# Optimization experiments

Hardware: AMD Instinct MI355X
Metric: run time of the kernel (lower is better)

Reference implementation:

```python
import jax, jax.numpy as jnp
import numpy as np

FILTER_LENGTH = 800
HOP_LENGTH = 200
WIN_LENGTH = 800
NUM_SAMPLES = 8_000_000


def _make_forward_basis():
    # Real/imag DFT rows (cutoff = N/2+1) times a periodic Hamming window.
    fl, wl = FILTER_LENGTH, WIN_LENGTH
    fourier = np.fft.fft(np.eye(fl))
    cutoff = fl // 2 + 1  # 401
    basis = np.vstack([fourier[:cutoff].real, fourier[:cutoff].imag])  # [802, 800]
    n = np.arange(wl)
    window = 0.54 - 0.46 * np.cos(2.0 * np.pi * n / wl)  # scipy get_window('hamming', wl, fftbins=True)
    basis = basis * window[None, :]
    return jnp.asarray(basis[:, None, :], dtype=jnp.float32)  # [802, 1, 800] (OIH)


def setup_inputs() -> dict:
    key = jax.random.key(0)
    input_data = jax.random.normal(key, (NUM_SAMPLES,), dtype=jnp.float32)
    forward_basis = _make_forward_basis()
    return {"input_data": input_data, "forward_basis": forward_basis}


def reference(input_data, forward_basis):
    fl, hop = FILTER_LENGTH, HOP_LENGTH
    cutoff = fl // 2 + 1
    x = input_data.reshape(1, 1, -1)  # (N=1, C=1, T)
    x = jnp.pad(x, ((0, 0), (0, 0), (fl // 2, fl // 2)), mode='reflect')
    # Strided conv with the dense DFT basis == framed windowed DFT.
    out = jax.lax.conv_general_dilated(
        x, forward_basis, window_strides=(hop,), padding='VALID',
        dimension_numbers=('NCH', 'OIH', 'NCH'))  # [1, 802, n_frames]
    real = out[:, :cutoff, :]
    imag = out[:, cutoff:, :]
    magnitude = jnp.sqrt(real * real + imag * imag)  # [1, 401, n_frames]
    return magnitude
```

## Files before the change

kernel.cpp:

```cpp
#include <hip/hip_runtime.h>


#define FL   800
#define HOP  200
#define CUT  401
#define NS   8000000
#define NT   40001
#define KSTEPS 25

#define FT   64
#define TT   384
#define NTT  105
#define SLICE_SH 77824
#define XBN  8016000
#define BB_OFF 16032000

typedef short short8 __attribute__((ext_vector_type(8)));
typedef float float4v __attribute__((ext_vector_type(4)));

#define GU32 const __attribute__((address_space(1))) unsigned int*
#define LU32 __attribute__((address_space(3))) unsigned int*

__device__ inline unsigned short f2bf(float f) {
    union { float f; unsigned u; } v; v.f = f;
    unsigned r = v.u + 0x7FFFu + ((v.u >> 16) & 1u);
    return (unsigned short)(r >> 16);
}

__global__ void prep_x(const float* __restrict__ x, short* __restrict__ xb) {
    const int n8 = XBN / 8;
    for (int j = blockIdx.x * blockDim.x + threadIdx.x; j < n8;
         j += gridDim.x * blockDim.x) {
        const int i = j * 8;
        const int s = i - 400;
        short8 o;
        if (s >= 0 && s + 7 < NS) {
            const float4v a = *reinterpret_cast<const float4v*>(x + s);
            const float4v b = *reinterpret_cast<const float4v*>(x + s + 4);
            o[0]=f2bf(a[0]); o[1]=f2bf(a[1]); o[2]=f2bf(a[2]); o[3]=f2bf(a[3]);
            o[4]=f2bf(b[0]); o[5]=f2bf(b[1]); o[6]=f2bf(b[2]); o[7]=f2bf(b[3]);
        } else {
            #pragma unroll
            for (int q = 0; q < 8; ++q) {
                int sq = s + q;
                if (sq < 0) sq = -sq;
                else if (sq >= NS) sq = 2 * NS - 2 - sq;
                o[q] = f2bf(x[sq]);
            }
        }
        *reinterpret_cast<short8*>(xb + i) = o;
    }
}

__global__ void prep_b(const float* __restrict__ basis, short* __restrict__ bb) {
    const int nch = 896 * 100;
    for (int j = blockIdx.x * blockDim.x + threadIdx.x; j < nch;
         j += gridDim.x * blockDim.x) {
        const int row = j / 100;
        const int col = (j % 100) * 8;
        short8 o;
        int src = -1;
        if (row < CUT) src = row;
        else if (row >= 448 && row < 448 + CUT) src = row - 47;
        if (src >= 0) {
            const float* p = basis + (size_t)src * 800 + col;
            const float4v a = *reinterpret_cast<const float4v*>(p);
            const float4v b = *reinterpret_cast<const float4v*>(p + 4);
            o[0]=f2bf(a[0]); o[1]=f2bf(a[1]); o[2]=f2bf(a[2]); o[3]=f2bf(a[3]);
            o[4]=f2bf(b[0]); o[5]=f2bf(b[1]); o[6]=f2bf(b[2]); o[7]=f2bf(b[3]);
        } else {
            #pragma unroll
            for (int q = 0; q < 8; ++q) o[q] = 0;
        }
        *reinterpret_cast<short8*>(bb + (size_t)row * 800 + col) = o;
    }
}

#define MF(A, X, C) C = __builtin_amdgcn_mfma_f32_16x16x32_bf16((A), (X), (C), 0, 0, 0)

#define BODY(KS, CA, CX, NA, NX)                                               \
  {                                                                            \
    if ((KS) < 24) {                                                           \
      NA[0] = *reinterpret_cast<const short8*>(pr0 + ((KS)+1)*32);             \
      NA[1] = *reinterpret_cast<const short8*>(pr1 + ((KS)+1)*32);             \
      NA[2] = *reinterpret_cast<const short8*>(pi0 + ((KS)+1)*32);             \
      NA[3] = *reinterpret_cast<const short8*>(pi1 + ((KS)+1)*32);             \
      NX[0] = *reinterpret_cast<const short8*>(&sX[xoff + 0*3200 + ((KS)+1)*32]); \
      NX[1] = *reinterpret_cast<const short8*>(&sX[xoff + 1*3200 + ((KS)+1)*32]); \
      NX[2] = *reinterpret_cast<const short8*>(&sX[xoff + 2*3200 + ((KS)+1)*32]); \
      NX[3] = *reinterpret_cast<const short8*>(&sX[xoff + 3*3200 + ((KS)+1)*32]); \
      NX[4] = *reinterpret_cast<const short8*>(&sX[xoff + 4*3200 + ((KS)+1)*32]); \
      NX[5] = *reinterpret_cast<const short8*>(&sX[xoff + 5*3200 + ((KS)+1)*32]); \
    }                                                                          \
    __builtin_amdgcn_s_setprio(1);                                             \
    MF(CA[0], CX[0], acc_r[0][0]); MF(CA[0], CX[1], acc_r[0][1]);              \
    MF(CA[0], CX[2], acc_r[0][2]); MF(CA[0], CX[3], acc_r[0][3]);              \
    MF(CA[0], CX[4], acc_r[0][4]); MF(CA[0], CX[5], acc_r[0][5]);              \
    MF(CA[1], CX[0], acc_r[1][0]); MF(CA[1], CX[1], acc_r[1][1]);              \
    MF(CA[1], CX[2], acc_r[1][2]); MF(CA[1], CX[3], acc_r[1][3]);              \
    MF(CA[1], CX[4], acc_r[1][4]); MF(CA[1], CX[5], acc_r[1][5]);              \
    MF(CA[2], CX[0], acc_i[0][0]); MF(CA[2], CX[1], acc_i[0][1]);              \
    MF(CA[2], CX[2], acc_i[0][2]); MF(CA[2], CX[3], acc_i[0][3]);              \
    MF(CA[2], CX[4], acc_i[0][4]); MF(CA[2], CX[5], acc_i[0][5]);              \
    MF(CA[3], CX[0], acc_i[1][0]); MF(CA[3], CX[1], acc_i[1][1]);              \
    MF(CA[3], CX[2], acc_i[1][2]); MF(CA[3], CX[3], acc_i[1][3]);              \
    MF(CA[3], CX[4], acc_i[1][4]); MF(CA[3], CX[5], acc_i[1][5]);              \
    __builtin_amdgcn_s_setprio(0);                                             \
  }

__global__ __launch_bounds__(512, 2)
void stft_mag_kernel(const short* __restrict__ xb,
                     const short* __restrict__ bb,
                     float* __restrict__ out) {
    __shared__ short sX[SLICE_SH];

    const int tid = threadIdx.x;

    const int nwg = NTT * 7;
    const int q = nwg >> 3, r = nwg & 7;
    const int bid = blockIdx.x;
    const int xcd = bid & 7, idx = bid >> 3;
    const int wgid = (xcd < r ? xcd * (q + 1) : r * (q + 1) + (xcd - r) * q) + idx;
    const int t0 = (wgid / 7) * TT;
    const int f0 = (wgid % 7) * FT;

    const int lane = tid & 63;
    const int wid  = tid >> 6;
    const int wm   = wid >> 2;
    const int wn   = wid & 3;
    const int l15  = lane & 15;
    const int l4   = lane >> 4;

    {
        const int g0 = t0 * HOP + tid * 8;
        short* dst = sX + tid * 8;
        #pragma unroll
        for (int it = 0; it < 19; ++it) {
            int off = g0 + it * 4096;
            if (off > XBN - 8) off = XBN - 8;
            __builtin_amdgcn_global_load_lds((GU32)(xb + off),
                                             (LU32)(dst + it * 4096), 16, 0, 0);
        }
    }

    const short* pr0 = bb + (size_t)(f0 + wm * 32 + l15) * 800 + l4 * 8;
    const short* pr1 = bb + (size_t)(f0 + wm * 32 + 16 + l15) * 800 + l4 * 8;
    const short* pi0 = pr0 + (size_t)448 * 800;
    const short* pi1 = pr1 + (size_t)448 * 800;

    const int xoff = (wn * 96 + l15) * HOP + l4 * 8;

    float4v acc_r[2][6] = {};
    float4v acc_i[2][6] = {};

    short8 FAa[4], FAx[6], FBa[4], FBx[6];

    FAa[0] = *reinterpret_cast<const short8*>(pr0);
    FAa[1] = *reinterpret_cast<const short8*>(pr1);
    FAa[2] = *reinterpret_cast<const short8*>(pi0);
    FAa[3] = *reinterpret_cast<const short8*>(pi1);

    asm volatile("s_waitcnt vmcnt(0)" ::: "memory");
    __builtin_amdgcn_s_barrier();
    asm volatile("" ::: "memory");

    FAx[0] = *reinterpret_cast<const short8*>(&sX[xoff + 0*3200]);
    FAx[1] = *reinterpret_cast<const short8*>(&sX[xoff + 1*3200]);
    FAx[2] = *reinterpret_cast<const short8*>(&sX[xoff + 2*3200]);
    FAx[3] = *reinterpret_cast<const short8*>(&sX[xoff + 3*3200]);
    FAx[4] = *reinterpret_cast<const short8*>(&sX[xoff + 4*3200]);
    FAx[5] = *reinterpret_cast<const short8*>(&sX[xoff + 5*3200]);

    #pragma unroll
    for (int jj = 0; jj < 12; ++jj) {
        BODY(2*jj,     FAa, FAx, FBa, FBx);
        BODY(2*jj + 1, FBa, FBx, FAa, FAx);
    }
    BODY(24, FAa, FAx, FBa, FBx);

    #pragma unroll
    for (int mi = 0; mi < 2; ++mi) {
        #pragma unroll
        for (int rr = 0; rr < 4; ++rr) {
            const int f = f0 + wm * 32 + mi * 16 + l4 * 4 + rr;
            if (f >= CUT) continue;
            #pragma unroll
            for (int ni = 0; ni < 6; ++ni) {
                const int t = t0 + wn * 96 + ni * 16 + l15;
                if (t < NT) {
                    const float vr = (mi == 0 ? acc_r[0][ni][rr] : acc_r[1][ni][rr]);
                    const float vi = (mi == 0 ? acc_i[0][ni][rr] : acc_i[1][ni][rr]);
                    out[(size_t)f * NT + t] = sqrtf(vr * vr + vi * vi);
                }
            }
        }
    }
}

extern "C" void kernel_launch(void* const* d_in, const int* in_sizes, int n_in,
                              void* d_out, int out_size, void* d_ws, size_t ws_size,
                              hipStream_t stream) {
    const float* x     = (const float*)d_in[0];
    const float* basis = (const float*)d_in[1];
    float* out = (float*)d_out;

    short* xb = (short*)d_ws;
    short* bb = (short*)((char*)d_ws + BB_OFF);

    prep_x<<<2048, 256, 0, stream>>>(x, xb);
    prep_b<<<350, 256, 0, stream>>>(basis, bb);

    stft_mag_kernel<<<NTT * 7, 512, 0, stream>>>(xb, bb, out);
}
```

Baseline: 77.72 us.

## Switch to 32x32x16 MFMA and halve time tile to 192 frames

Replaces the 16x16x32 bf16 MFMA tiles with 32x32x16 MFMAs, so each wave computes 32 frequencies by 96 frames using three accumulators per real/imag part. The time tile shrinks to 192 frames per 256-thread block, which doubles the grid and halves the LDS slice. The larger MFMA shape cuts the instruction count and the register fragment traffic per flop. In exchange, each block loads relatively more overlapping input per frame, and K-chunks are now read from LDS in two 16-element halves.

```diff
diff --git a/kernel.cpp b/kernel.cpp
--- a/kernel.cpp
+++ b/kernel.cpp
@@ -9,14 +9,15 @@
 #define KSTEPS 25
 
 #define FT   64
-#define TT   384
-#define NTT  105
-#define SLICE_SH 77824
+#define TT   192
+#define NTT  209
+#define SLICE_SH 40000
 #define XBN  8016000
 #define BB_OFF 16032000
 
 typedef short short8 __attribute__((ext_vector_type(8)));
 typedef float float4v __attribute__((ext_vector_type(4)));
+typedef float f32x16 __attribute__((ext_vector_type(16)));
 
 #define GU32 const __attribute__((address_space(1))) unsigned int*
 #define LU32 __attribute__((address_space(3))) unsigned int*
@@ -76,39 +77,35 @@
     }
 }
 
-#define MF(A, X, C) C = __builtin_amdgcn_mfma_f32_16x16x32_bf16((A), (X), (C), 0, 0, 0)
+#define MF32(A, X, C) C = __builtin_amdgcn_mfma_f32_32x32x16_bf16((A), (X), (C), 0, 0, 0)
 
 #define BODY(KS, CA, CX, NA, NX)                                               \
   {                                                                            \
     if ((KS) < 24) {                                                           \
-      NA[0] = *reinterpret_cast<const short8*>(pr0 + ((KS)+1)*32);             \
-      NA[1] = *reinterpret_cast<const short8*>(pr1 + ((KS)+1)*32);             \
-      NA[2] = *reinterpret_cast<const short8*>(pi0 + ((KS)+1)*32);             \
-      NA[3] = *reinterpret_cast<const short8*>(pi1 + ((KS)+1)*32);             \
-      NX[0] = *reinterpret_cast<const short8*>(&sX[xoff + 0*3200 + ((KS)+1)*32]); \
-      NX[1] = *reinterpret_cast<const short8*>(&sX[xoff + 1*3200 + ((KS)+1)*32]); \
-      NX[2] = *reinterpret_cast<const short8*>(&sX[xoff + 2*3200 + ((KS)+1)*32]); \
-      NX[3] = *reinterpret_cast<const short8*>(&sX[xoff + 3*3200 + ((KS)+1)*32]); \
-      NX[4] = *reinterpret_cast<const short8*>(&sX[xoff + 4*3200 + ((KS)+1)*32]); \
-      NX[5] = *reinterpret_cast<const short8*>(&sX[xoff + 5*3200 + ((KS)+1)*32]); \
+      NA[0] = *reinterpret_cast<const short8*>(par + ((KS)+1)*32);             \
+      NA[1] = *reinterpret_cast<const short8*>(par + ((KS)+1)*32 + 16);        \
+      NA[2] = *reinterpret_cast<const short8*>(pai + ((KS)+1)*32);             \
+      NA[3] = *reinterpret_cast<const short8*>(pai + ((KS)+1)*32 + 16);        \
+      NX[0] = *reinterpret_cast<const short8*>(&sX[xoff + 0*6400 + ((KS)+1)*32]);      \
+      NX[1] = *reinterpret_cast<const short8*>(&sX[xoff + 0*6400 + ((KS)+1)*32 + 16]); \
+      NX[2] = *reinterpret_cast<const short8*>(&sX[xoff + 1*6400 + ((KS)+1)*32]);      \
+      NX[3] = *reinterpret_cast<const short8*>(&sX[xoff + 1*6400 + ((KS)+1)*32 + 16]); \
+      NX[4] = *reinterpret_cast<const short8*>(&sX[xoff + 2*6400 + ((KS)+1)*32]);      \
+      NX[5] = *reinterpret_cast<const short8*>(&sX[xoff + 2*6400 + ((KS)+1)*32 + 16]); \
     }                                                                          \
     __builtin_amdgcn_s_setprio(1);                                             \
-    MF(CA[0], CX[0], acc_r[0][0]); MF(CA[0], CX[1], acc_r[0][1]);              \
-    MF(CA[0], CX[2], acc_r[0][2]); MF(CA[0], CX[3], acc_r[0][3]);              \
-    MF(CA[0], CX[4], acc_r[0][4]); MF(CA[0], CX[5], acc_r[0][5]);              \
-    MF(CA[1], CX[0], acc_r[1][0]); MF(CA[1], CX[1], acc_r[1][1]);              \
-    MF(CA[1], CX[2], acc_r[1][2]); MF(CA[1], CX[3], acc_r[1][3]);              \
-    MF(CA[1], CX[4], acc_r[1][4]); MF(CA[1], CX[5], acc_r[1][5]);              \
-    MF(CA[2], CX[0], acc_i[0][0]); MF(CA[2], CX[1], acc_i[0][1]);              \
-    MF(CA[2], CX[2], acc_i[0][2]); MF(CA[2], CX[3], acc_i[0][3]);              \
-    MF(CA[2], CX[4], acc_i[0][4]); MF(CA[2], CX[5], acc_i[0][5]);              \
-    MF(CA[3], CX[0], acc_i[1][0]); MF(CA[3], CX[1], acc_i[1][1]);              \
-    MF(CA[3], CX[2], acc_i[1][2]); MF(CA[3], CX[3], acc_i[1][3]);              \
-    MF(CA[3], CX[4], acc_i[1][4]); MF(CA[3], CX[5], acc_i[1][5]);              \
+    MF32(CA[0], CX[0], acc_r[0]); MF32(CA[0], CX[2], acc_r[1]);                \
+    MF32(CA[0], CX[4], acc_r[2]);                                              \
+    MF32(CA[2], CX[0], acc_i[0]); MF32(CA[2], CX[2], acc_i[1]);                \
+    MF32(CA[2], CX[4], acc_i[2]);                                              \
+    MF32(CA[1], CX[1], acc_r[0]); MF32(CA[1], CX[3], acc_r[1]);                \
+    MF32(CA[1], CX[5], acc_r[2]);                                              \
+    MF32(CA[3], CX[1], acc_i[0]); MF32(CA[3], CX[3], acc_i[1]);                \
+    MF32(CA[3], CX[5], acc_i[2]);                                              \
     __builtin_amdgcn_s_setprio(0);                                             \
   }
 
-__global__ __launch_bounds__(512, 2)
+__global__ __launch_bounds__(256, 2)
 void stft_mag_kernel(const short* __restrict__ xb,
                      const short* __restrict__ bb,
                      float* __restrict__ out) {
@@ -126,50 +123,54 @@
 
     const int lane = tid & 63;
     const int wid  = tid >> 6;
-    const int wm   = wid >> 2;
-    const int wn   = wid & 3;
-    const int l15  = lane & 15;
-    const int l4   = lane >> 4;
+    const int wm   = wid >> 1;
+    const int wn   = wid & 1;
+    const int l31  = lane & 31;
+    const int lk   = lane >> 5;
 
     {
         const int g0 = t0 * HOP + tid * 8;
         short* dst = sX + tid * 8;
         #pragma unroll
         for (int it = 0; it < 19; ++it) {
-            int off = g0 + it * 4096;
+            int off = g0 + it * 2048;
             if (off > XBN - 8) off = XBN - 8;
             __builtin_amdgcn_global_load_lds((GU32)(xb + off),
-                                             (LU32)(dst + it * 4096), 16, 0, 0);
-        }
-    }
-
-    const short* pr0 = bb + (size_t)(f0 + wm * 32 + l15) * 800 + l4 * 8;
-    const short* pr1 = bb + (size_t)(f0 + wm * 32 + 16 + l15) * 800 + l4 * 8;
-    const short* pi0 = pr0 + (size_t)448 * 800;
-    const short* pi1 = pr1 + (size_t)448 * 800;
-
-    const int xoff = (wn * 96 + l15) * HOP + l4 * 8;
-
-    float4v acc_r[2][6] = {};
-    float4v acc_i[2][6] = {};
+                                             (LU32)(dst + it * 2048), 16, 0, 0);
+        }
+        if (tid < 136) {
+            int off = g0 + 19 * 2048;
+            if (off > XBN - 8) off = XBN - 8;
+            __builtin_amdgcn_global_load_lds((GU32)(xb + off),
+                                             (LU32)(dst + 19 * 2048), 16, 0, 0);
+        }
+    }
+
+    const short* par = bb + (size_t)(f0 + wm * 32 + l31) * 800 + lk * 8;
+    const short* pai = par + (size_t)448 * 800;
+
+    const int xoff = (wn * 96 + l31) * 200 + lk * 8;
+
+    f32x16 acc_r[3] = {};
+    f32x16 acc_i[3] = {};
 
     short8 FAa[4], FAx[6], FBa[4], FBx[6];
 
-    FAa[0] = *reinterpret_cast<const short8*>(pr0);
-    FAa[1] = *reinterpret_cast<const short8*>(pr1);
-    FAa[2] = *reinterpret_cast<const short8*>(pi0);
-    FAa[3] = *reinterpret_cast<const short8*>(pi1);
+    FAa[0] = *reinterpret_cast<const short8*>(par);
+    FAa[1] = *reinterpret_cast<const short8*>(par + 16);
+    FAa[2] = *reinterpret_cast<const short8*>(pai);
+    FAa[3] = *reinterpret_cast<const short8*>(pai + 16);
 
     asm volatile("s_waitcnt vmcnt(0)" ::: "memory");
     __builtin_amdgcn_s_barrier();
     asm volatile("" ::: "memory");
 
-    FAx[0] = *reinterpret_cast<const short8*>(&sX[xoff + 0*3200]);
-    FAx[1] = *reinterpret_cast<const short8*>(&sX[xoff + 1*3200]);
-    FAx[2] = *reinterpret_cast<const short8*>(&sX[xoff + 2*3200]);
-    FAx[3] = *reinterpret_cast<const short8*>(&sX[xoff + 3*3200]);
-    FAx[4] = *reinterpret_cast<const short8*>(&sX[xoff + 4*3200]);
-    FAx[5] = *reinterpret_cast<const short8*>(&sX[xoff + 5*3200]);
+    FAx[0] = *reinterpret_cast<const short8*>(&sX[xoff + 0*6400]);
+    FAx[1] = *reinterpret_cast<const short8*>(&sX[xoff + 0*6400 + 16]);
+    FAx[2] = *reinterpret_cast<const short8*>(&sX[xoff + 1*6400]);
+    FAx[3] = *reinterpret_cast<const short8*>(&sX[xoff + 1*6400 + 16]);
+    FAx[4] = *reinterpret_cast<const short8*>(&sX[xoff + 2*6400]);
+    FAx[5] = *reinterpret_cast<const short8*>(&sX[xoff + 2*6400 + 16]);
 
     #pragma unroll
     for (int jj = 0; jj < 12; ++jj) {
@@ -179,17 +180,16 @@
     BODY(24, FAa, FAx, FBa, FBx);
 
     #pragma unroll
-    for (int mi = 0; mi < 2; ++mi) {
-        #pragma unroll
-        for (int rr = 0; rr < 4; ++rr) {
-            const int f = f0 + wm * 32 + mi * 16 + l4 * 4 + rr;
-            if (f >= CUT) continue;
+    for (int ni = 0; ni < 3; ++ni) {
+        const int t = t0 + wn * 96 + ni * 32 + l31;
+        if (t < NT) {
             #pragma unroll
-            for (int ni = 0; ni < 6; ++ni) {
-                const int t = t0 + wn * 96 + ni * 16 + l15;
-                if (t < NT) {
-                    const float vr = (mi == 0 ? acc_r[0][ni][rr] : acc_r[1][ni][rr]);
-                    const float vi = (mi == 0 ? acc_i[0][ni][rr] : acc_i[1][ni][rr]);
+            for (int reg = 0; reg < 16; ++reg) {
+                const int row = (reg & 3) + 8 * (reg >> 2) + 4 * lk;
+                const int f = f0 + wm * 32 + row;
+                if (f < CUT) {
+                    const float vr = acc_r[ni][reg];
+                    const float vi = acc_i[ni][reg];
                     out[(size_t)f * NT + t] = sqrtf(vr * vr + vi * vi);
                 }
             }
@@ -210,5 +210,5 @@
     prep_x<<<2048, 256, 0, stream>>>(x, xb);
     prep_b<<<350, 256, 0, stream>>>(basis, bb);
 
-    stft_mag_kernel<<<NTT * 7, 512, 0, stream>>>(xb, bb, out);
-}
+    stft_mag_kernel<<<NTT * 7, 256, 0, stream>>>(xb, bb, out);
+}
```

Result: slower. 81.69 us (+5.1%).
